# Performance work log

Hardware: AMD Instinct MI355X
Metric: run time of the kernel (lower is better)

## Reference

```python
import jax, jax.numpy as jnp
import numpy as np

DIM = 1024
NUM_EXPERTS = 8
HIDDEN = 4096
CAP_FACTOR = 2.0
B, S = 4, 2048


def setup_inputs() -> dict:
    key = jax.random.key(0)
    ks = jax.random.split(key, 6)
    scale_r = 1.0 / np.sqrt(DIM)
    scale_1 = 1.0 / np.sqrt(DIM)
    scale_2 = 1.0 / np.sqrt(HIDDEN)
    return {
        "x": jax.random.normal(ks[0], (B, S, DIM), dtype=jnp.float32),
        # router: nn.Linear(dim, num_experts, bias=False) -> weight [E, D]
        "router_w": jax.random.uniform(ks[1], (NUM_EXPERTS, DIM), jnp.float32, -scale_r, scale_r),
        # stacked expert MLP params
        "w1": jax.random.uniform(ks[2], (NUM_EXPERTS, DIM, HIDDEN), jnp.float32, -scale_1, scale_1),
        "b1": jax.random.uniform(ks[3], (NUM_EXPERTS, HIDDEN), jnp.float32, -scale_1, scale_1),
        "w2": jax.random.uniform(ks[4], (NUM_EXPERTS, HIDDEN, DIM), jnp.float32, -scale_2, scale_2),
        "b2": jax.random.uniform(ks[5], (NUM_EXPERTS, DIM), jnp.float32, -scale_2, scale_2),
    }


def reference(x, router_w, w1, b1, w2, b2):
    # x: [B, S, D]
    Bz, Sz, Dz = x.shape
    E = router_w.shape[0]
    capacity = max(1, int(Sz * CAP_FACTOR / E) + 1)

    # router softmax over experts: [B, S, E]
    scores = jax.nn.softmax(jnp.einsum("bsd,ed->bse", x, router_w), axis=-1)

    # expert-choice: each expert picks top-C tokens. [B, E, S] -> [B, E, C]
    scores_t = jnp.swapaxes(scores, 1, 2)
    gate_vals, sel_idx = jax.lax.top_k(scores_t, capacity)

    # gather selected tokens: [B, E, C, D]
    b_idx = jnp.arange(Bz)[:, None, None]
    tokens = x[b_idx, sel_idx]

    # batched expert MLP (GELU exact, matching nn.GELU default)
    h = jnp.einsum("becd,edh->bech", tokens, w1) + b1[None, :, None, :]
    h = jax.nn.gelu(h, approximate=False)
    y = jnp.einsum("bech,ehd->becd", h, w2) + b2[None, :, None, :]

    # gate and scatter-add combine back to [B, S, D]
    gated = y * gate_vals[..., None]
    out = jnp.zeros_like(x).at[b_idx, sel_idx].add(gated)
    return out
```

## Files before the change

kernel.cpp:

```cpp
#include <hip/hip_runtime.h>
#include <cstdint>

#define DIMD  1024
#define NEXP  8
#define HIDN  4096
#define BATCH 4
#define SEQ   2048
#define CAPC  513
#define RPEX  2176
#define TPEX  17
#define MTOT  (NEXP * RPEX)
#define MTILES (MTOT / 128)

typedef __bf16 bf16x8 __attribute__((ext_vector_type(8)));
typedef float  f32x4  __attribute__((ext_vector_type(4)));

__device__ __forceinline__ unsigned short f2bf(float f) {
    unsigned u = __float_as_uint(f);
    unsigned r = (u + 0x7FFFu + ((u >> 16) & 1u)) >> 16;
    return (unsigned short)r;
}

__device__ __forceinline__ void gl16(const unsigned short* g, unsigned short* l) {
    __builtin_amdgcn_global_load_lds(
        (const __attribute__((address_space(1))) void*)g,
        (__attribute__((address_space(3))) void*)l, 16, 0, 0);
}

__device__ __forceinline__ void swz_grp(int GY, int& bx, int& by) {
    int xcd = blockIdx.x & 7, pos = blockIdx.x >> 3;
    int tps = TPEX * GY;
    int sc = pos / tps, rem = pos - sc * tps;
    int bxl = rem / GY, byIn = rem - bxl * GY;
    bx = xcd * TPEX + bxl;
    by = sc * GY + byIn;
}

__global__ __launch_bounds__(64)
void router_kernel(const float* __restrict__ x, const float* __restrict__ rw,
                   float* __restrict__ scores) {
    int token = blockIdx.x;
    int lane  = threadIdx.x;
    const float4* xr = reinterpret_cast<const float4*>(x + (size_t)token * DIMD);
    float4 xv[4];
#pragma unroll
    for (int j = 0; j < 4; ++j) xv[j] = xr[lane * 4 + j];
    float acc[NEXP];
#pragma unroll
    for (int e = 0; e < NEXP; ++e) {
        const float4* wr = reinterpret_cast<const float4*>(rw + (size_t)e * DIMD);
        float a = 0.f;
#pragma unroll
        for (int j = 0; j < 4; ++j) {
            float4 wv = wr[lane * 4 + j];
            a += xv[j].x * wv.x; a += xv[j].y * wv.y;
            a += xv[j].z * wv.z; a += xv[j].w * wv.w;
        }
#pragma unroll
        for (int off = 32; off > 0; off >>= 1) a += __shfl_xor(a, off);
        acc[e] = a;
    }
    float m = acc[0];
#pragma unroll
    for (int e = 1; e < NEXP; ++e) m = fmaxf(m, acc[e]);
    float s = 0.f;
#pragma unroll
    for (int e = 0; e < NEXP; ++e) { acc[e] = expf(acc[e] - m); s += acc[e]; }
    float inv = 1.f / s;
    if (lane == 0) {
        int b = token >> 11;
        int t = token & (SEQ - 1);
#pragma unroll
        for (int e = 0; e < NEXP; ++e)
            scores[((size_t)(b * NEXP + e)) * SEQ + t] = acc[e] * inv;
    }
}

__global__ __launch_bounds__(256)
void topk_kernel(const float* __restrict__ scores, int* __restrict__ sel,
                 float* __restrict__ gate, int* __restrict__ cnt,
                 int* __restrict__ invmap) {
    int be    = blockIdx.x >> 3;
    int chunk = blockIdx.x & 7;
    const float* sc = scores + (size_t)be * SEQ;
    __shared__ float s_sc[SEQ];
    int t = threadIdx.x;
#pragma unroll
    for (int q = 0; q < 8; ++q) s_sc[t + q * 256] = sc[t + q * 256];
    __syncthreads();
    int i = chunk * 256 + t;
    float v = s_sc[i];
    int r = 0;
#pragma unroll 8
    for (int j = 0; j < SEQ; ++j) {
        float u = s_sc[j];
        r += (u > v) || (u == v && j < i);
    }
    if (r < CAPC) {
        sel [(size_t)be * CAPC + r] = i;
        gate[(size_t)be * CAPC + r] = v;
        int b = be >> 3, e = be & 7;
        int tok = b * SEQ + i;
        int p = atomicAdd(cnt + tok, 1);
        invmap[(size_t)tok * 8 + p] = e * RPEX + b * CAPC + r;
    }
}

__global__ __launch_bounds__(256)
void gather_kernel(const float* __restrict__ x, const int* __restrict__ sel,
                   unsigned short* __restrict__ dhi) {
    int gr = blockIdx.x;
    int e  = gr / RPEX;
    int rl = gr - e * RPEX;
    int t  = threadIdx.x;
    size_t dbase = (size_t)gr * DIMD + t * 4;
    if (rl < BATCH * CAPC) {
        int b = rl / CAPC, c = rl - b * CAPC;
        int tok = sel[(size_t)(b * NEXP + e) * CAPC + c];
        float4 v = *reinterpret_cast<const float4*>(x + ((size_t)(b * SEQ + tok)) * DIMD + t * 4);
        ushort4 h;
        h.x = f2bf(v.x); h.y = f2bf(v.y); h.z = f2bf(v.z); h.w = f2bf(v.w);
        *reinterpret_cast<ushort4*>(dhi + dbase) = h;
    } else {
        ushort4 z = {0, 0, 0, 0};
        *reinterpret_cast<ushort4*>(dhi + dbase) = z;
    }
}

__global__ __launch_bounds__(256)
void convT_kernel(const float* __restrict__ src, unsigned short* __restrict__ dhi,
                  int Nsrc, size_t srcEStride, int k0, int n0, int kLen, int nLen) {
    int e = blockIdx.z;
    src += (size_t)e * srcEStride;
    dhi += (size_t)e * kLen * nLen;
    int kb = blockIdx.x * 64, nb = blockIdx.y * 64;
    __shared__ float T[64][65];
    int t = threadIdx.x;
    for (int i = t; i < 1024; i += 256) {
        int r = i >> 4, c4 = (i & 15) * 4;
        float4 v = *reinterpret_cast<const float4*>(
            src + (size_t)(k0 + kb + r) * Nsrc + n0 + nb + c4);
        T[r][c4 + 0] = v.x; T[r][c4 + 1] = v.y; T[r][c4 + 2] = v.z; T[r][c4 + 3] = v.w;
    }
    __syncthreads();
    for (int i = t; i < 1024; i += 256) {
        int n = i >> 4, kc = (i & 15) * 4;
        ushort4 h;
        h.x = f2bf(T[kc + 0][n]); h.y = f2bf(T[kc + 1][n]);
        h.z = f2bf(T[kc + 2][n]); h.w = f2bf(T[kc + 3][n]);
        *reinterpret_cast<ushort4*>(dhi + (size_t)(nb + n) * kLen + kb + kc) = h;
    }
}


#define GEMM_PRE(Abase, Bbase, Kc)                                              \
    int t = threadIdx.x;                                                        \
    int l = t & 63, wid = t >> 6;                                               \
    int wr = wid >> 1, wc = wid & 1;                                            \
    int grp = l >> 4, li = l & 15;                                              \
    int fsw  = (grp ^ ((li >> 1) & 3)) * 8;         \
    int gsrc = ((l & 3) ^ ((l >> 3) & 3)) * 8;      \
    int ra0 = (wid * 2) * 16 + (l >> 2);          \
    int ra1 = ra0 + 16;                                                         \
    __shared__ __align__(16) unsigned short As[2][4096];                        \
    __shared__ __align__(16) unsigned short Bs[2][4096];                        \
    int regA = wid * 1024;                            \
    const unsigned short* gA0 = (Abase) + (size_t)(bx * 128 + ra0) * (Kc) + gsrc; \
    const unsigned short* gA1 = (Abase) + (size_t)(bx * 128 + ra1) * (Kc) + gsrc; \
    const unsigned short* gB0 = (Bbase) + (size_t)(bn + ra0) * (Kc) + gsrc;     \
    const unsigned short* gB1 = (Bbase) + (size_t)(bn + ra1) * (Kc) + gsrc;     \
    f32x4 acc[4][4];                                                            \
    _Pragma("unroll")                                                           \
    for (int m = 0; m < 4; ++m)                                                 \
        _Pragma("unroll")                                                       \
        for (int n = 0; n < 4; ++n) { f32x4 z = {0.f,0.f,0.f,0.f}; acc[m][n] = z; }

#define STAGE(buf, kt) do {                                                     \
    gl16(gA0 + (kt), &As[buf][regA]);                                           \
    gl16(gA1 + (kt), &As[buf][regA + 512]);                                     \
    gl16(gB0 + (kt), &Bs[buf][regA]);                                           \
    gl16(gB1 + (kt), &Bs[buf][regA + 512]); } while (0)

#define GEMM_LOOP(Kc) do {                                                      \
    STAGE(0, 0);                                                                \
    __syncthreads();                                                            \
    int cur = 0;                                                                \
    for (int kt = 0; kt < (Kc); kt += 32) {                                     \
        if (kt + 32 < (Kc)) STAGE(cur ^ 1, kt + 32);                            \
        bf16x8 ah[4], bh[4];                                                    \
        const unsigned short* aB = &As[cur][wr * 2048 + li * 32 + fsw];         \
        const unsigned short* bB = &Bs[cur][wc * 2048 + li * 32 + fsw];         \
        ah[0] = *(const bf16x8*)(aB);        ah[1] = *(const bf16x8*)(aB + 512); \
        ah[2] = *(const bf16x8*)(aB + 1024); ah[3] = *(const bf16x8*)(aB + 1536); \
        bh[0] = *(const bf16x8*)(bB);        bh[1] = *(const bf16x8*)(bB + 512); \
        bh[2] = *(const bf16x8*)(bB + 1024); bh[3] = *(const bf16x8*)(bB + 1536); \
        _Pragma("unroll")                                                       \
        for (int m = 0; m < 4; ++m)                                             \
            _Pragma("unroll")                                                   \
            for (int n = 0; n < 4; ++n)                                         \
                acc[m][n] = __builtin_amdgcn_mfma_f32_16x16x32_bf16(            \
                    ah[m], bh[n], acc[m][n], 0, 0, 0);                          \
        __syncthreads();                                                        \
        cur ^= 1;                                                               \
    } } while (0)

__global__ __launch_bounds__(256)
void gemm1_mfma(const unsigned short* __restrict__ Ahi,
                const unsigned short* __restrict__ Whi,
                const float* __restrict__ bias, unsigned short* __restrict__ Hhi,
                size_t wstride, int nbias0, int ldh, int GY) {
    const int K = DIMD;
    int bx, by; swz_grp(GY, bx, by);
    int bn = by * 128;
    int e = bx / TPEX;
    const unsigned short* Bh = Whi + (size_t)e * wstride;

    GEMM_PRE(Ahi, Bh, K)
    GEMM_LOOP(K);

    int hr0 = bx * 128 + wr * 64;
    int cb = bn + wc * 64;
#pragma unroll
    for (int m = 0; m < 4; ++m)
#pragma unroll
        for (int q = 0; q < 4; ++q) {
            int row = hr0 + m * 16 + grp * 4 + q;
#pragma unroll
            for (int n = 0; n < 4; ++n) {
                int col = cb + n * 16 + li;
                float v = acc[m][n][q] + bias[(size_t)e * HIDN + nbias0 + col];
                float g = 0.5f * v * (1.0f + erff(v * 0.70710678118654752f));
                Hhi[(size_t)row * ldh + col] = f2bf(g);
            }
        }
}

__global__ __launch_bounds__(256)
void gemm2_mfma(const unsigned short* __restrict__ Ahi,
                const unsigned short* __restrict__ Whi,
                const float* __restrict__ bias, const float* __restrict__ gate,
                float* __restrict__ Y, size_t wstride, int K, int GY) {
    int bx, by; swz_grp(GY, bx, by);
    int bn = by * 128;
    int e = bx / TPEX;
    int rbase_e = (bx - e * TPEX) * 128;
    const unsigned short* Bh = Whi + (size_t)e * wstride;

    GEMM_PRE(Ahi, Bh, K)
    GEMM_LOOP(K);

    int cb = bn + wc * 64;
#pragma unroll
    for (int m = 0; m < 4; ++m)
#pragma unroll
        for (int q = 0; q < 4; ++q) {
            int off = wr * 64 + m * 16 + grp * 4 + q;
            int rloc = rbase_e + off;
            if (rloc < BATCH * CAPC) {
                int b = rloc / CAPC, c = rloc - b * CAPC;
                float g = gate[(size_t)(b * NEXP + e) * CAPC + c];
                size_t grow = (size_t)bx * 128 + off;
#pragma unroll
                for (int n = 0; n < 4; ++n) {
                    int col = cb + n * 16 + li;
                    float v = acc[m][n][q];
                    size_t yo = grow * DIMD + col;
                    if (bias) Y[yo] = g * (v + bias[(size_t)e * DIMD + col]);
                    else      Y[yo] = Y[yo] + g * v;
                }
            }
        }
}

__global__ __launch_bounds__(64)
void combine_kernel(const float* __restrict__ Y, const int* __restrict__ cnt,
                    const int* __restrict__ invmap, float* __restrict__ out) {
    int tok = blockIdx.x;
    int lane = threadIdx.x;
    int n = cnt[tok];
    f32x4 acc[4];
#pragma unroll
    for (int q = 0; q < 4; ++q) { f32x4 z = {0.f, 0.f, 0.f, 0.f}; acc[q] = z; }
#pragma unroll
    for (int j = 0; j < 8; ++j) {
        if (j < n) {
            int row = invmap[(size_t)tok * 8 + j];
            const f32x4* yr = reinterpret_cast<const f32x4*>(Y + (size_t)row * DIMD);
#pragma unroll
            for (int q = 0; q < 4; ++q) acc[q] += yr[q * 64 + lane];
        }
    }
    f32x4* op = reinterpret_cast<f32x4*>(out + (size_t)tok * DIMD);
#pragma unroll
    for (int q = 0; q < 4; ++q) op[q * 64 + lane] = acc[q];
}

extern "C" void kernel_launch(void* const* d_in, const int* in_sizes, int n_in,
                              void* d_out, int out_size, void* d_ws, size_t ws_size,
                              hipStream_t stream) {
    (void)in_sizes; (void)n_in; (void)out_size;
    const float* x  = (const float*)d_in[0];
    const float* rw = (const float*)d_in[1];
    const float* w1 = (const float*)d_in[2];
    const float* b1 = (const float*)d_in[3];
    const float* w2 = (const float*)d_in[4];
    const float* b2 = (const float*)d_in[5];
    float* out = (float*)d_out;

    char* ws = (char*)d_ws;
    size_t off = 0;
    auto alloc = [&](size_t bytes) -> char* {
        char* p = ws + off;
        off = (off + bytes + 255) & ~(size_t)255;
        return p;
    };

    float* scores = (float*)alloc((size_t)BATCH * NEXP * SEQ * 4);
    int*   sel    = (int*)  alloc((size_t)BATCH * NEXP * CAPC * 4);
    float* gate   = (float*)alloc((size_t)BATCH * NEXP * CAPC * 4);
    int*   cnt    = (int*)  alloc((size_t)BATCH * SEQ * 4);
    int*   invmap = (int*)  alloc((size_t)BATCH * SEQ * 8 * 4);
    float* Y      = (float*)alloc((size_t)MTOT * DIMD * 4);
    size_t common = off;

    const size_t A1B = (size_t)MTOT * DIMD * 2;
    int C = 8;
    for (int c = 1; c <= 8; c <<= 1) {
        size_t wc = (size_t)NEXP * (HIDN / c) * DIMD * 2;
        size_t hc = (size_t)MTOT * (HIDN / c) * 2;
        size_t need = common + A1B + 2 * wc + hc + (8u << 20);
        if (need <= ws_size) { C = c; break; }
    }
    const int HN = HIDN / C;
    const int nY1 = HN / 128;
    const int GY1 = (nY1 < 8) ? nY1 : 8;

    unsigned short* A1h = (unsigned short*)alloc(A1B);
    size_t WCB = (size_t)NEXP * HN * DIMD * 2;
    size_t HCB = (size_t)MTOT * HN * 2;
    unsigned short* W1h = (unsigned short*)alloc(WCB);
    unsigned short* W2h = (unsigned short*)alloc(WCB);
    unsigned short* Hh  = (unsigned short*)alloc(HCB);

    hipMemsetAsync(cnt, 0, (size_t)BATCH * SEQ * 4, stream);
    router_kernel<<<BATCH * SEQ, 64, 0, stream>>>(x, rw, scores);
    topk_kernel<<<BATCH * NEXP * 8, 256, 0, stream>>>(scores, sel, gate, cnt, invmap);
    gather_kernel<<<MTOT, 256, 0, stream>>>(x, sel, A1h);

    for (int c = 0; c < C; ++c) {
        convT_kernel<<<dim3(DIMD / 64, HN / 64, NEXP), 256, 0, stream>>>(
            w1, W1h, HIDN, (size_t)DIMD * HIDN, 0, c * HN, DIMD, HN);
        gemm1_mfma<<<MTILES * nY1, 256, 0, stream>>>(
            A1h, W1h, b1, Hh, (size_t)HN * DIMD, c * HN, HN, GY1);
        convT_kernel<<<dim3(HN / 64, DIMD / 64, NEXP), 256, 0, stream>>>(
            w2, W2h, DIMD, (size_t)HIDN * DIMD, c * HN, 0, HN, DIMD);
        gemm2_mfma<<<MTILES * (DIMD / 128), 256, 0, stream>>>(
            Hh, W2h, (c == 0) ? b2 : nullptr, gate, Y,
            (size_t)DIMD * HN, HN, 4);
    }
    combine_kernel<<<BATCH * SEQ, 64, 0, stream>>>(Y, cnt, invmap, out);
}
```

Baseline: 650.9 us.

## Replace gemm1 with 256x256-tile triple-buffered MFMA kernel and faster GELU

The first expert GEMM now uses 512-thread blocks computing 256x256 output tiles instead of 128x128, raising reuse of each loaded tile. Operands move through a three-stage LDS ring with explicit vmcnt waits, and A/B loads are interleaved with MFMA phases under s_setprio. To make 256-row tiles fit, the per-expert row padding grows from 2176 to 2304, which adds wasted padded rows to gemm2 as well. The exact erf GELU is replaced by a tanh-style approximation built from exp2 and rcp, trading some accuracy for cheaper epilogue math.

```diff
diff --git a/kernel.cpp b/kernel.cpp
--- a/kernel.cpp
+++ b/kernel.cpp
@@ -7,10 +7,12 @@
 #define BATCH 4
 #define SEQ   2048
 #define CAPC  513
-#define RPEX  2176
-#define TPEX  17
+#define RPEX  2304
+#define TPEX  18
+#define TP256 9
 #define MTOT  (NEXP * RPEX)
 #define MTILES (MTOT / 128)
+#define MT256  (MTOT / 256)
 
 typedef __bf16 bf16x8 __attribute__((ext_vector_type(8)));
 typedef float  f32x4  __attribute__((ext_vector_type(4)));
@@ -152,19 +154,135 @@
     }
 }
 
+__global__ __launch_bounds__(512, 2)
+void gemm1_8ph(const unsigned short* __restrict__ A,
+               const unsigned short* __restrict__ W,
+               const float* __restrict__ bias, unsigned short* __restrict__ Hhi,
+               size_t wstride, int nbias0, int ldh, int GY) {
+    const int K = DIMD;
+    const int NT = K / 32;
+
+    int xcd = blockIdx.x & 7, pos = blockIdx.x >> 3;
+    int tps = TP256 * GY;
+    int sc = pos / tps, rem = pos - sc * tps;
+    int bxl = rem / GY, byIn = rem - bxl * GY;
+    int bx = xcd * TP256 + bxl;
+    int by = sc * GY + byIn;
+    int bn = by * 256;
+    int e = bx / TP256;
+    const unsigned short* B = W + (size_t)e * wstride;
+
+    int t = threadIdx.x;
+    int l = t & 63, wid = t >> 6;
+    int wr = wid >> 2, wc = wid & 3;
+    int grp = l >> 4, li = l & 15;
+
+    __shared__ __align__(16) unsigned short Ab[3][8192];
+    __shared__ __align__(16) unsigned short Bb[3][8192];
+
+    int sr = t >> 2, sq = t & 3;
+    int qs = (sq ^ ((sr >> 1) & 3)) * 8;
+    const unsigned short* gA0 = A + (size_t)(bx * 256 + sr) * K + qs;
+    const unsigned short* gA1 = A + (size_t)(bx * 256 + 128 + sr) * K + qs;
+    const unsigned short* gB0 = B + (size_t)(bn + sr) * K + qs;
+    const unsigned short* gB1 = B + (size_t)(bn + 128 + sr) * K + qs;
+    int ldsw = wid * 512;
+
+#define ST_A(bf, tt) do { gl16(gA0 + (tt) * 32, &Ab[bf][ldsw]);        \
+                          gl16(gA1 + (tt) * 32, &Ab[bf][4096 + ldsw]); } while (0)
+#define ST_B(bf, tt) do { gl16(gB0 + (tt) * 32, &Bb[bf][ldsw]);        \
+                          gl16(gB1 + (tt) * 32, &Bb[bf][4096 + ldsw]); } while (0)
+
+    f32x4 acc[8][4];
+#pragma unroll
+    for (int m = 0; m < 8; ++m)
+#pragma unroll
+        for (int n = 0; n < 4; ++n) { f32x4 z = {0.f, 0.f, 0.f, 0.f}; acc[m][n] = z; }
+
+    int fsw  = (grp ^ ((li >> 1) & 3)) * 8;
+    int aoff = wr * 4096 + li * 32 + fsw;
+    int boff = (wc >> 1) * 4096 + ((wc & 1) * 64 + li) * 32 + fsw;
+
+    ST_A(0, 0); ST_B(0, 0);
+    ST_A(1, 1); ST_B(1, 1);
+
+    int cb = 0;
+    for (int tt = 0; tt < NT; ++tt) {
+        if (tt == NT - 1) asm volatile("s_waitcnt vmcnt(0)" ::: "memory");
+        else              asm volatile("s_waitcnt vmcnt(4)" ::: "memory");
+        __builtin_amdgcn_s_barrier();
+
+        int sb = cb + 2; if (sb >= 3) sb -= 3;
+        const unsigned short* ab = &Ab[cb][0];
+        const unsigned short* bb = &Bb[cb][0];
+
+        if (tt + 2 < NT) ST_A(sb, tt + 2);
+        bf16x8 bf[4], af[4];
+#pragma unroll
+        for (int n = 0; n < 4; ++n) bf[n] = *(const bf16x8*)(bb + boff + n * 512);
+#pragma unroll
+        for (int m = 0; m < 4; ++m) af[m] = *(const bf16x8*)(ab + aoff + m * 512);
+        __builtin_amdgcn_s_setprio(1);
+#pragma unroll
+        for (int m = 0; m < 4; ++m)
+#pragma unroll
+            for (int n = 0; n < 4; ++n)
+                acc[m][n] = __builtin_amdgcn_mfma_f32_16x16x32_bf16(
+                    af[m], bf[n], acc[m][n], 0, 0, 0);
+        __builtin_amdgcn_s_setprio(0);
+
+        if (tt + 2 < NT) ST_B(sb, tt + 2);
+#pragma unroll
+        for (int m = 0; m < 4; ++m)
+            af[m] = *(const bf16x8*)(ab + aoff + (m + 4) * 512);
+        __builtin_amdgcn_s_setprio(1);
+#pragma unroll
+        for (int m = 0; m < 4; ++m)
+#pragma unroll
+            for (int n = 0; n < 4; ++n)
+                acc[m + 4][n] = __builtin_amdgcn_mfma_f32_16x16x32_bf16(
+                    af[m], bf[n], acc[m + 4][n], 0, 0, 0);
+        __builtin_amdgcn_s_setprio(0);
+
+        ++cb; if (cb == 3) cb = 0;
+    }
+#undef ST_A
+#undef ST_B
+
+    float bs[4];
+#pragma unroll
+    for (int n = 0; n < 4; ++n)
+        bs[n] = bias[(size_t)e * HIDN + nbias0 + bn + wc * 64 + n * 16 + li];
+    const float cc0 = 0.044715f;
+    const float cc1 = -2.302118131f;
+#pragma unroll
+    for (int m = 0; m < 8; ++m)
+#pragma unroll
+        for (int q = 0; q < 4; ++q) {
+            int row = bx * 256 + wr * 128 + m * 16 + grp * 4 + q;
+#pragma unroll
+            for (int n = 0; n < 4; ++n) {
+                int col = bn + wc * 64 + n * 16 + li;
+                float v = acc[m][n][q] + bs[n];
+                float p = __builtin_fmaf(cc0 * v, v * v, v);
+                float g = v * __builtin_amdgcn_rcpf(1.0f + exp2f(cc1 * p));
+                Hhi[(size_t)row * ldh + col] = f2bf(g);
+            }
+        }
+}
 
 #define GEMM_PRE(Abase, Bbase, Kc)                                              \
     int t = threadIdx.x;                                                        \
     int l = t & 63, wid = t >> 6;                                               \
     int wr = wid >> 1, wc = wid & 1;                                            \
     int grp = l >> 4, li = l & 15;                                              \
-    int fsw  = (grp ^ ((li >> 1) & 3)) * 8;         \
-    int gsrc = ((l & 3) ^ ((l >> 3) & 3)) * 8;      \
-    int ra0 = (wid * 2) * 16 + (l >> 2);          \
+    int fsw  = (grp ^ ((li >> 1) & 3)) * 8;                                     \
+    int gsrc = ((l & 3) ^ ((l >> 3) & 3)) * 8;                                  \
+    int ra0 = (wid * 2) * 16 + (l >> 2);                                        \
     int ra1 = ra0 + 16;                                                         \
     __shared__ __align__(16) unsigned short As[2][4096];                        \
     __shared__ __align__(16) unsigned short Bs[2][4096];                        \
-    int regA = wid * 1024;                            \
+    int regA = wid * 1024;                                                      \
     const unsigned short* gA0 = (Abase) + (size_t)(bx * 128 + ra0) * (Kc) + gsrc; \
     const unsigned short* gA1 = (Abase) + (size_t)(bx * 128 + ra1) * (Kc) + gsrc; \
     const unsigned short* gB0 = (Bbase) + (size_t)(bn + ra0) * (Kc) + gsrc;     \
@@ -205,37 +323,6 @@
     } } while (0)
 
 __global__ __launch_bounds__(256)
-void gemm1_mfma(const unsigned short* __restrict__ Ahi,
-                const unsigned short* __restrict__ Whi,
-                const float* __restrict__ bias, unsigned short* __restrict__ Hhi,
-                size_t wstride, int nbias0, int ldh, int GY) {
-    const int K = DIMD;
-    int bx, by; swz_grp(GY, bx, by);
-    int bn = by * 128;
-    int e = bx / TPEX;
-    const unsigned short* Bh = Whi + (size_t)e * wstride;
-
-    GEMM_PRE(Ahi, Bh, K)
-    GEMM_LOOP(K);
-
-    int hr0 = bx * 128 + wr * 64;
-    int cb = bn + wc * 64;
-#pragma unroll
-    for (int m = 0; m < 4; ++m)
-#pragma unroll
-        for (int q = 0; q < 4; ++q) {
-            int row = hr0 + m * 16 + grp * 4 + q;
-#pragma unroll
-            for (int n = 0; n < 4; ++n) {
-                int col = cb + n * 16 + li;
-                float v = acc[m][n][q] + bias[(size_t)e * HIDN + nbias0 + col];
-                float g = 0.5f * v * (1.0f + erff(v * 0.70710678118654752f));
-                Hhi[(size_t)row * ldh + col] = f2bf(g);
-            }
-        }
-}
-
-__global__ __launch_bounds__(256)
 void gemm2_mfma(const unsigned short* __restrict__ Ahi,
                 const unsigned short* __restrict__ Whi,
                 const float* __restrict__ bias, const float* __restrict__ gate,
@@ -332,8 +419,8 @@
         if (need <= ws_size) { C = c; break; }
     }
     const int HN = HIDN / C;
-    const int nY1 = HN / 128;
-    const int GY1 = (nY1 < 8) ? nY1 : 8;
+    const int nY256 = HN / 256;
+    const int GY1 = (nY256 < 8) ? nY256 : 8;
 
     unsigned short* A1h = (unsigned short*)alloc(A1B);
     size_t WCB = (size_t)NEXP * HN * DIMD * 2;
@@ -350,7 +437,7 @@
     for (int c = 0; c < C; ++c) {
         convT_kernel<<<dim3(DIMD / 64, HN / 64, NEXP), 256, 0, stream>>>(
             w1, W1h, HIDN, (size_t)DIMD * HIDN, 0, c * HN, DIMD, HN);
-        gemm1_mfma<<<MTILES * nY1, 256, 0, stream>>>(
+        gemm1_8ph<<<MT256 * nY256, 512, 0, stream>>>(
             A1h, W1h, b1, Hh, (size_t)HN * DIMD, c * HN, HN, GY1);
         convT_kernel<<<dim3(HN / 64, DIMD / 64, NEXP), 256, 0, stream>>>(
             w2, W2h, DIMD, (size_t)HIDN * DIMD, c * HN, 0, HN, DIMD);
```

New measurement: 651.1 us. About the same (+0.0%).

## Triple-buffer GEMM LDS pipeline with vmcnt waits and use tanh-form GELU

Applied to the files above, without the earlier changes.

The GEMM K-loop now uses three LDS stages with two tiles prefetched ahead. It waits with explicit s_waitcnt vmcnt plus one barrier per iteration instead of two __syncthreads, and raises wave priority around the MFMA block. This aims to hide global-to-LDS latency and cut sync overhead, at the cost of 50% more shared memory, which may reduce occupancy. The exact erf GELU epilogue is also replaced by the tanh approximation computed via exp2 and rcp, which is cheaper but deviates slightly from the exact GELU the reference specifies.

```diff
diff --git a/kernel.cpp b/kernel.cpp
--- a/kernel.cpp
+++ b/kernel.cpp
@@ -158,13 +158,13 @@
     int l = t & 63, wid = t >> 6;                                               \
     int wr = wid >> 1, wc = wid & 1;                                            \
     int grp = l >> 4, li = l & 15;                                              \
-    int fsw  = (grp ^ ((li >> 1) & 3)) * 8;         \
-    int gsrc = ((l & 3) ^ ((l >> 3) & 3)) * 8;      \
-    int ra0 = (wid * 2) * 16 + (l >> 2);          \
+    int fsw  = (grp ^ ((li >> 1) & 3)) * 8;                                     \
+    int gsrc = ((l & 3) ^ ((l >> 3) & 3)) * 8;                                  \
+    int ra0 = (wid * 2) * 16 + (l >> 2);                                        \
     int ra1 = ra0 + 16;                                                         \
-    __shared__ __align__(16) unsigned short As[2][4096];                        \
-    __shared__ __align__(16) unsigned short Bs[2][4096];                        \
-    int regA = wid * 1024;                            \
+    __shared__ __align__(16) unsigned short As[3][4096];                        \
+    __shared__ __align__(16) unsigned short Bs[3][4096];                        \
+    int regA = wid * 1024;                                                      \
     const unsigned short* gA0 = (Abase) + (size_t)(bx * 128 + ra0) * (Kc) + gsrc; \
     const unsigned short* gA1 = (Abase) + (size_t)(bx * 128 + ra1) * (Kc) + gsrc; \
     const unsigned short* gB0 = (Bbase) + (size_t)(bn + ra0) * (Kc) + gsrc;     \
@@ -182,26 +182,32 @@
     gl16(gB1 + (kt), &Bs[buf][regA + 512]); } while (0)
 
 #define GEMM_LOOP(Kc) do {                                                      \
+    const int NT = (Kc) / 32;                                                   \
     STAGE(0, 0);                                                                \
-    __syncthreads();                                                            \
-    int cur = 0;                                                                \
-    for (int kt = 0; kt < (Kc); kt += 32) {                                     \
-        if (kt + 32 < (Kc)) STAGE(cur ^ 1, kt + 32);                            \
+    STAGE(1, 32);                                                               \
+    int cb = 0;                                                                 \
+    for (int tt = 0; tt < NT; ++tt) {                                           \
+        if (tt == NT - 1) asm volatile("s_waitcnt vmcnt(0)" ::: "memory");      \
+        else              asm volatile("s_waitcnt vmcnt(4)" ::: "memory");      \
+        __builtin_amdgcn_s_barrier();                                           \
+        int sb = cb + 2; if (sb >= 3) sb -= 3;                                  \
+        if (tt + 2 < NT) STAGE(sb, (tt + 2) * 32);                              \
         bf16x8 ah[4], bh[4];                                                    \
-        const unsigned short* aB = &As[cur][wr * 2048 + li * 32 + fsw];         \
-        const unsigned short* bB = &Bs[cur][wc * 2048 + li * 32 + fsw];         \
+        const unsigned short* aB = &As[cb][wr * 2048 + li * 32 + fsw];          \
+        const unsigned short* bB = &Bs[cb][wc * 2048 + li * 32 + fsw];          \
         ah[0] = *(const bf16x8*)(aB);        ah[1] = *(const bf16x8*)(aB + 512); \
         ah[2] = *(const bf16x8*)(aB + 1024); ah[3] = *(const bf16x8*)(aB + 1536); \
         bh[0] = *(const bf16x8*)(bB);        bh[1] = *(const bf16x8*)(bB + 512); \
         bh[2] = *(const bf16x8*)(bB + 1024); bh[3] = *(const bf16x8*)(bB + 1536); \
+        __builtin_amdgcn_s_setprio(1);                                          \
         _Pragma("unroll")                                                       \
         for (int m = 0; m < 4; ++m)                                             \
             _Pragma("unroll")                                                   \
             for (int n = 0; n < 4; ++n)                                         \
                 acc[m][n] = __builtin_amdgcn_mfma_f32_16x16x32_bf16(            \
                     ah[m], bh[n], acc[m][n], 0, 0, 0);                          \
-        __syncthreads();                                                        \
-        cur ^= 1;                                                               \
+        __builtin_amdgcn_s_setprio(0);                                          \
+        ++cb; if (cb == 3) cb = 0;                                              \
     } } while (0)
 
 __global__ __launch_bounds__(256)
@@ -219,7 +225,9 @@
     GEMM_LOOP(K);
 
     int hr0 = bx * 128 + wr * 64;
-    int cb = bn + wc * 64;
+    int cb2 = bn + wc * 64;
+    const float cc0 = 0.044715f;
+    const float cc1 = -2.302118131f;
 #pragma unroll
     for (int m = 0; m < 4; ++m)
 #pragma unroll
@@ -227,9 +235,10 @@
             int row = hr0 + m * 16 + grp * 4 + q;
 #pragma unroll
             for (int n = 0; n < 4; ++n) {
-                int col = cb + n * 16 + li;
+                int col = cb2 + n * 16 + li;
                 float v = acc[m][n][q] + bias[(size_t)e * HIDN + nbias0 + col];
-                float g = 0.5f * v * (1.0f + erff(v * 0.70710678118654752f));
+                float p = __builtin_fmaf(cc0 * v, v * v, v);
+                float g = v * __builtin_amdgcn_rcpf(1.0f + exp2f(cc1 * p));
                 Hhi[(size_t)row * ldh + col] = f2bf(g);
             }
         }
@@ -249,7 +258,7 @@
     GEMM_PRE(Ahi, Bh, K)
     GEMM_LOOP(K);
 
-    int cb = bn + wc * 64;
+    int cb2 = bn + wc * 64;
 #pragma unroll
     for (int m = 0; m < 4; ++m)
 #pragma unroll
@@ -262,7 +271,7 @@
                 size_t grow = (size_t)bx * 128 + off;
 #pragma unroll
                 for (int n = 0; n < 4; ++n) {
-                    int col = cb + n * 16 + li;
+                    int col = cb2 + n * 16 + li;
                     float v = acc[m][n][q];
                     size_t yo = grow * DIMD + col;
                     if (bias) Y[yo] = g * (v + bias[(size_t)e * DIMD + col]);
```

After: 619.6 us. -4.8%, faster.
